# Optimization experiments

Hardware: AMD Instinct MI355X
Metric: run time of the kernel (lower is better)

The kernel has to match this reference:

```python
import jax, jax.numpy as jnp
import numpy as np

B, N, D_IN, D, E, MAXD = 16, 512, 256, 64, 32, 50
LN_EPS = 1e-5

def setup_inputs() -> dict:
    key = jax.random.key(0)
    ks = jax.random.split(key, 24)
    s = lambda fan: 1.0 / np.sqrt(fan)
    inp = {
        'x': jax.random.normal(ks[0], (B, N, D_IN), jnp.float32),
        'price_rising_ranks': jax.random.randint(ks[1], (B, N), 0, N, jnp.int64),
        'Wp': jax.random.normal(ks[2], (D_IN, D), jnp.float32) * s(D_IN),
        'bp': jnp.zeros((D,), jnp.float32),
        'Wq': jax.random.normal(ks[3], (D, D), jnp.float32) * s(D),
        'bq': jnp.zeros((D,), jnp.float32),
        'Wk': jax.random.normal(ks[4], (D, D), jnp.float32) * s(D),
        'bk': jnp.zeros((D,), jnp.float32),
        'Wv': jax.random.normal(ks[5], (D, D), jnp.float32) * s(D),
        'bv': jnp.zeros((D,), jnp.float32),
        'Eemb': jax.random.normal(ks[6], (MAXD + 1, E), jnp.float32),
        'Wr1': jax.random.normal(ks[7], (E, 16), jnp.float32) * s(E),
        'br1': jnp.zeros((16,), jnp.float32),
        'Wr2': jax.random.normal(ks[8], (16, 1), jnp.float32) * s(16),
        'Wf1': jax.random.normal(ks[9], (D, 2 * D), jnp.float32) * s(D),
        'bf1': jnp.zeros((2 * D,), jnp.float32),
        'Wf2': jax.random.normal(ks[10], (2 * D, D), jnp.float32) * s(2 * D),
        'bf2': jnp.zeros((D,), jnp.float32),
        'ln_g': jnp.ones((D,), jnp.float32),
        'ln_b': jnp.zeros((D,), jnp.float32),
        'Ws1': jax.random.normal(ks[11], (D, 32), jnp.float32) * s(D),
        'bs1': jnp.zeros((32,), jnp.float32),
        'Ws2': jax.random.normal(ks[12], (32, 1), jnp.float32) * s(32),
        'bs2': jnp.zeros((1,), jnp.float32),
    }
    return inp

def reference(x, price_rising_ranks, Wp, bp, Wq, bq, Wk, bk, Wv, bv,
              Eemb, Wr1, br1, Wr2, Wf1, bf1, Wf2, bf2, ln_g, ln_b,
              Ws1, bs1, Ws2, bs2):
    xp = x @ Wp + bp                                  # (B,N,D)
    q = xp @ Wq + bq
    k = xp @ Wk + bk
    v = xp @ Wv + bv
    scores = jnp.einsum('bnd,bmd->bnm', q, k) / jnp.sqrt(jnp.float32(D))
    # rank-distance pairwise bias
    r = price_rising_ranks
    dists = jnp.clip(jnp.abs(r[:, :, None] - r[:, None, :]), 0, MAXD)  # (B,N,N) int
    emb = Eemb[dists]                                 # (B,N,N,E)
    w = jax.nn.relu(emb @ Wr1 + br1) @ Wr2            # (B,N,N,1)
    rel = jax.nn.sigmoid(w[..., 0])                   # (B,N,N)
    scores = scores * rel
    attn = jax.nn.softmax(scores, axis=-1)
    ao = jnp.einsum('bnm,bmd->bnd', attn, v)
    # feed forward + layernorm
    h = jax.nn.relu(ao @ Wf1 + bf1) @ Wf2 + bf2
    mu = jnp.mean(h, axis=-1, keepdims=True)
    var = jnp.mean((h - mu) ** 2, axis=-1, keepdims=True)
    hn = (h - mu) / jnp.sqrt(var + LN_EPS) * ln_g + ln_b
    # score projection
    out = jax.nn.relu(hn @ Ws1 + bs1) @ Ws2 + bs2     # (B,N,1)
    return jax.nn.sigmoid(out[..., 0])                # (B,N)
```

## Files before the change

### kernel.cpp

```cpp
#include <hip/hip_runtime.h>

using f32x4 = __attribute__((ext_vector_type(4))) float;
using s16x8 = __attribute__((ext_vector_type(8))) short;

static __device__ __forceinline__ unsigned short f2bf(float f){
  union { float f; unsigned int i; } c; c.f = f;
  return (unsigned short)((c.i + 0x7FFFu + ((c.i >> 16) & 1u)) >> 16);
}
static __device__ __forceinline__ s16x8 ld8(const unsigned short* p){
  return *(const s16x8*)p;
}
static __device__ __forceinline__ s16x8 cvt8(const float* p){
  const float4* q = (const float4*)p;
  float4 a = q[0], b = q[1];
  s16x8 r;
  r[0]=(short)f2bf(a.x); r[1]=(short)f2bf(a.y); r[2]=(short)f2bf(a.z); r[3]=(short)f2bf(a.w);
  r[4]=(short)f2bf(b.x); r[5]=(short)f2bf(b.y); r[6]=(short)f2bf(b.z); r[7]=(short)f2bf(b.w);
  return r;
}
static __device__ __forceinline__ f32x4 mfma16(s16x8 a, s16x8 b, f32x4 c){
  return __builtin_amdgcn_mfma_f32_16x16x32_bf16(a, b, c, 0, 0, 0);
}

__global__ __launch_bounds__(128) void k_proj(const float* __restrict__ x,
    const float* __restrict__ Wp, const float* __restrict__ bp,
    const float* __restrict__ Wq, const float* __restrict__ bq,
    const float* __restrict__ Wk, const float* __restrict__ bk,
    const float* __restrict__ Wv, const float* __restrict__ bv,
    const float* __restrict__ Ee, const float* __restrict__ Wr1,
    const float* __restrict__ br1, const float* __restrict__ Wr2,
    unsigned short* __restrict__ q, unsigned short* __restrict__ kk,
    unsigned short* __restrict__ vt, float* __restrict__ rel_t)
{
  __shared__ __align__(16) unsigned short WpT[64*264];
  __shared__ __align__(16) unsigned short Wt3[3][64*72];
  __shared__ __align__(16) unsigned short xs[2][16*72];

  int t = threadIdx.x;
  for (int i = t; i < 256*64; i += 128){
    int k = i >> 6, n = i & 63;
    WpT[n*264 + k] = f2bf(Wp[i]);
  }
  for (int i = t; i < 64*64; i += 128){
    int k2 = i >> 6, n = i & 63;
    Wt3[0][n*72 + k2] = f2bf(Wq[i]);
    Wt3[1][n*72 + k2] = f2bf(Wk[i]);
    Wt3[2][n*72 + k2] = f2bf(Wv[i]);
  }
  if (blockIdx.x == 0 && t < 51){
    float e[32];
    for (int j = 0; j < 32; ++j) e[j] = Ee[t*32 + j];
    float w = 0.f;
    for (int h = 0; h < 16; ++h){
      float s = br1[h];
      for (int j = 0; j < 32; ++j) s += e[j] * Wr1[j*16 + h];
      w += fmaxf(s, 0.f) * Wr2[h];
    }
    rel_t[t] = 1.f / (1.f + __expf(-w));
  }
  __syncthreads();

  int lane = t & 63, wave = t >> 6, colL = lane & 15, quad = lane >> 4;
  int row0 = blockIdx.x*32 + wave*16;

  const float* xr = x + (row0 + colL)*256;
  f32x4 acc[4] = {};
  for (int kc = 0; kc < 256; kc += 32){
    s16x8 a = cvt8(xr + kc + quad*8);
#pragma unroll
    for (int nt = 0; nt < 4; ++nt)
      acc[nt] = mfma16(a, ld8(&WpT[(nt*16+colL)*264 + kc + quad*8]), acc[nt]);
  }
  unsigned short* xw = xs[wave];
#pragma unroll
  for (int nt = 0; nt < 4; ++nt){
    int col = nt*16 + colL;
    float bb = bp[col];
#pragma unroll
    for (int i = 0; i < 4; ++i)
      xw[(quad*4+i)*72 + col] = f2bf(acc[nt][i] + bb);
  }
  s16x8 a0 = ld8(&xw[colL*72 +  0 + quad*8]);
  s16x8 a1 = ld8(&xw[colL*72 + 32 + quad*8]);

#pragma unroll
  for (int w = 0; w < 3; ++w){
    const float* bias = w==0 ? bq : (w==1 ? bk : bv);
    f32x4 c[4] = {};
#pragma unroll
    for (int nt = 0; nt < 4; ++nt){
      c[nt] = mfma16(a0, ld8(&Wt3[w][(nt*16+colL)*72 +  0 + quad*8]), c[nt]);
      c[nt] = mfma16(a1, ld8(&Wt3[w][(nt*16+colL)*72 + 32 + quad*8]), c[nt]);
    }
#pragma unroll
    for (int nt = 0; nt < 4; ++nt){
      int col = nt*16 + colL;
      float bb = bias[col];
#pragma unroll
      for (int i = 0; i < 4; ++i){
        int row = row0 + quad*4 + i;
        float v = c[nt][i] + bb;
        if (w == 0)      q [row*64 + col] = f2bf(v);
        else if (w == 1) kk[row*64 + col] = f2bf(v);
        else             vt[(row>>9)*32768 + col*512 + (row & 511)] = f2bf(v);
      }
    }
  }
}

__global__ __launch_bounds__(256) void k_attn(const unsigned short* __restrict__ q,
    const unsigned short* __restrict__ kmat, const unsigned short* __restrict__ vt,
    const int* __restrict__ ranks, const float* __restrict__ rel_t,
    unsigned short* __restrict__ ao)
{
  int b = blockIdx.y, qt = blockIdx.x;
  int t = threadIdx.x, lane = t & 63, wave = t >> 6;
  int colL = lane & 15, quad = lane >> 4;

  __shared__ int r_s[512];
  __shared__ float rt_s[64];
  __shared__ __align__(16) unsigned short P[4][16*136];
  __shared__ float Opart[4][16*66];
  __shared__ float pmax_s[4][16], psum_s[4][16];

  for (int i = t; i < 512; i += 256) r_s[i] = ranks[b*512 + i];
  if (t < 64) rt_s[t] = (t < 51) ? rel_t[t] : 0.f;
  __syncthreads();

  int qrow0 = qt*16;
  const unsigned short* qp = q    + b*32768;
  const unsigned short* kp = kmat + b*32768;
  const unsigned short* vp = vt   + b*32768;

  s16x8 aq0 = ld8(qp + (qrow0+colL)*64 +  0 + quad*8);
  s16x8 aq1 = ld8(qp + (qrow0+colL)*64 + 32 + quad*8);

  int key0 = wave*128;
  f32x4 S[8];
#pragma unroll
  for (int mt = 0; mt < 8; ++mt){
    int key = key0 + mt*16 + colL;
    f32x4 c = {};
    c = mfma16(aq0, ld8(kp + key*64 +  0 + quad*8), c);
    c = mfma16(aq1, ld8(kp + key*64 + 32 + quad*8), c);
    S[mt] = c;
  }

  int rq[4];
#pragma unroll
  for (int i = 0; i < 4; ++i) rq[i] = r_s[qrow0 + quad*4 + i];

  float rmax[4] = {-1e30f,-1e30f,-1e30f,-1e30f};
#pragma unroll
  for (int mt = 0; mt < 8; ++mt){
    int rm = r_s[key0 + mt*16 + colL];
#pragma unroll
    for (int i = 0; i < 4; ++i){
      int dd = rq[i] - rm; dd = dd < 0 ? -dd : dd; dd = dd > 50 ? 50 : dd;
      float s = S[mt][i] * 0.125f * rt_s[dd];
      S[mt][i] = s;
      rmax[i] = fmaxf(rmax[i], s);
    }
  }
#pragma unroll
  for (int i = 0; i < 4; ++i){
    rmax[i] = fmaxf(rmax[i], __shfl_xor(rmax[i], 1));
    rmax[i] = fmaxf(rmax[i], __shfl_xor(rmax[i], 2));
    rmax[i] = fmaxf(rmax[i], __shfl_xor(rmax[i], 4));
    rmax[i] = fmaxf(rmax[i], __shfl_xor(rmax[i], 8));
  }
  if (colL == 0){
#pragma unroll
    for (int i = 0; i < 4; ++i) pmax_s[wave][quad*4 + i] = rmax[i];
  }
  __syncthreads();
  float gmax[4];
#pragma unroll
  for (int i = 0; i < 4; ++i){
    int r = quad*4 + i;
    gmax[i] = fmaxf(fmaxf(pmax_s[0][r], pmax_s[1][r]), fmaxf(pmax_s[2][r], pmax_s[3][r]));
  }
  float rsum[4] = {0.f,0.f,0.f,0.f};
#pragma unroll
  for (int mt = 0; mt < 8; ++mt){
#pragma unroll
    for (int i = 0; i < 4; ++i){
      float p = __expf(S[mt][i] - gmax[i]);
      S[mt][i] = p;
      rsum[i] += p;
    }
  }
#pragma unroll
  for (int i = 0; i < 4; ++i){
    rsum[i] += __shfl_xor(rsum[i], 1);
    rsum[i] += __shfl_xor(rsum[i], 2);
    rsum[i] += __shfl_xor(rsum[i], 4);
    rsum[i] += __shfl_xor(rsum[i], 8);
  }
  if (colL == 0){
#pragma unroll
    for (int i = 0; i < 4; ++i) psum_s[wave][quad*4 + i] = rsum[i];
  }
  __syncthreads();
  float inv[4];
#pragma unroll
  for (int i = 0; i < 4; ++i){
    int r = quad*4 + i;
    inv[i] = 1.f / (psum_s[0][r] + psum_s[1][r] + psum_s[2][r] + psum_s[3][r]);
  }
  unsigned short* Pw = P[wave];
#pragma unroll
  for (int mt = 0; mt < 8; ++mt){
#pragma unroll
    for (int i = 0; i < 4; ++i)
      Pw[(quad*4+i)*136 + mt*16 + colL] = f2bf(S[mt][i] * inv[i]);
  }
  f32x4 O[4] = {};
#pragma unroll
  for (int mc = 0; mc < 128; mc += 32){
    s16x8 ap = ld8(&Pw[colL*136 + mc + quad*8]);
#pragma unroll
    for (int dt = 0; dt < 4; ++dt)
      O[dt] = mfma16(ap, ld8(vp + (dt*16+colL)*512 + key0 + mc + quad*8), O[dt]);
  }
  float* Ow = Opart[wave];
#pragma unroll
  for (int dt = 0; dt < 4; ++dt)
#pragma unroll
    for (int i = 0; i < 4; ++i)
      Ow[(quad*4+i)*66 + dt*16 + colL] = O[dt][i];
  __syncthreads();
  for (int e = t; e < 1024; e += 256){
    int row = e >> 6, col = e & 63;
    float s = Opart[0][row*66+col] + Opart[1][row*66+col]
            + Opart[2][row*66+col] + Opart[3][row*66+col];
    ao[(b*512 + qrow0 + row)*64 + col] = f2bf(s);
  }
}

__global__ __launch_bounds__(128) void k_ffn(const unsigned short* __restrict__ ao,
    const float* __restrict__ Wf1, const float* __restrict__ bf1,
    const float* __restrict__ Wf2, const float* __restrict__ bf2,
    const float* __restrict__ lng, const float* __restrict__ lnb,
    const float* __restrict__ Ws1, const float* __restrict__ bs1,
    const float* __restrict__ Ws2, const float* __restrict__ bs2,
    float* __restrict__ out)
{
  __shared__ __align__(16) unsigned short Wf1t[128*72];
  __shared__ __align__(16) unsigned short Wf2t[64*136];
  __shared__ __align__(16) unsigned short Ws1t[32*72];
  __shared__ __align__(16) unsigned short hbuf[2][16*136];
  __shared__ float cb[384];

  int t = threadIdx.x;
  for (int i = t; i < 64*128; i += 128){ int d = i>>7, j = i&127; Wf1t[j*72 + d] = f2bf(Wf1[i]); }
  for (int i = t; i < 128*64; i += 128){ int kx = i>>6, n = i&63; Wf2t[n*136 + kx] = f2bf(Wf2[i]); }
  for (int i = t; i < 64*32;  i += 128){ int d = i>>5, c = i&31; Ws1t[c*72 + d] = f2bf(Ws1[i]); }
  if (t < 128) cb[t] = bf1[t];
  if (t < 64){ cb[128+t] = bf2[t]; cb[192+t] = lng[t]; cb[256+t] = lnb[t]; }
  if (t < 32){ cb[320+t] = bs1[t]; cb[352+t] = Ws2[t]; }
  __syncthreads();

  int lane = t & 63, wave = t >> 6, colL = lane & 15, quad = lane >> 4;
  int row0 = blockIdx.x*32 + wave*16;
  unsigned short* hw = hbuf[wave];

  f32x4 a1[8] = {};
#pragma unroll
  for (int kc = 0; kc < 64; kc += 32){
    s16x8 a = ld8(ao + (row0+colL)*64 + kc + quad*8);
#pragma unroll
    for (int nt = 0; nt < 8; ++nt)
      a1[nt] = mfma16(a, ld8(&Wf1t[(nt*16+colL)*72 + kc + quad*8]), a1[nt]);
  }
#pragma unroll
  for (int nt = 0; nt < 8; ++nt){
    int col = nt*16 + colL;
    float bb = cb[col];
#pragma unroll
    for (int i = 0; i < 4; ++i)
      hw[(quad*4+i)*136 + col] = f2bf(fmaxf(a1[nt][i] + bb, 0.f));
  }
  f32x4 a2[4] = {};
#pragma unroll
  for (int kc = 0; kc < 128; kc += 32){
    s16x8 a = ld8(&hw[colL*136 + kc + quad*8]);
#pragma unroll
    for (int nt = 0; nt < 4; ++nt)
      a2[nt] = mfma16(a, ld8(&Wf2t[(nt*16+colL)*136 + kc + quad*8]), a2[nt]);
  }
  float vals[4][4];
#pragma unroll
  for (int nt = 0; nt < 4; ++nt){
    float bb = cb[128 + nt*16 + colL];
#pragma unroll
    for (int i = 0; i < 4; ++i) vals[i][nt] = a2[nt][i] + bb;
  }
  float hnv[4][4];
#pragma unroll
  for (int i = 0; i < 4; ++i){
    float s = vals[i][0]+vals[i][1]+vals[i][2]+vals[i][3];
    s += __shfl_xor(s,1); s += __shfl_xor(s,2); s += __shfl_xor(s,4); s += __shfl_xor(s,8);
    float mu = s * (1.f/64.f);
    float d0=vals[i][0]-mu, d1=vals[i][1]-mu, d2=vals[i][2]-mu, d3=vals[i][3]-mu;
    float s2 = d0*d0 + d1*d1 + d2*d2 + d3*d3;
    s2 += __shfl_xor(s2,1); s2 += __shfl_xor(s2,2); s2 += __shfl_xor(s2,4); s2 += __shfl_xor(s2,8);
    float invs = rsqrtf(s2*(1.f/64.f) + 1e-5f);
#pragma unroll
    for (int nt = 0; nt < 4; ++nt){
      int col = nt*16 + colL;
      hnv[i][nt] = (vals[i][nt]-mu)*invs*cb[192+col] + cb[256+col];
    }
  }
#pragma unroll
  for (int i = 0; i < 4; ++i)
#pragma unroll
    for (int nt = 0; nt < 4; ++nt)
      hw[(quad*4+i)*72 + nt*16 + colL] = f2bf(hnv[i][nt]);

  f32x4 a3[2] = {};
#pragma unroll
  for (int kc = 0; kc < 64; kc += 32){
    s16x8 a = ld8(&hw[colL*72 + kc + quad*8]);
#pragma unroll
    for (int nt = 0; nt < 2; ++nt)
      a3[nt] = mfma16(a, ld8(&Ws1t[(nt*16+colL)*72 + kc + quad*8]), a3[nt]);
  }
  float bs2f = bs2[0];
#pragma unroll
  for (int i = 0; i < 4; ++i){
    float p = 0.f;
#pragma unroll
    for (int nt = 0; nt < 2; ++nt){
      int col = nt*16 + colL;
      p += fmaxf(a3[nt][i] + cb[320+col], 0.f) * cb[352+col];
    }
    p += __shfl_xor(p,1); p += __shfl_xor(p,2); p += __shfl_xor(p,4); p += __shfl_xor(p,8);
    if (colL == 0){
      float z = p + bs2f;
      out[row0 + quad*4 + i] = 1.f / (1.f + __expf(-z));
    }
  }
}

extern "C" void kernel_launch(void* const* d_in, const int* in_sizes, int n_in,
                              void* d_out, int out_size, void* d_ws, size_t ws_size,
                              hipStream_t stream)
{
  const float* x    = (const float*)d_in[0];
  const int*   rank = (const int*)d_in[1];
  const float* Wp   = (const float*)d_in[2];
  const float* bp   = (const float*)d_in[3];
  const float* Wq   = (const float*)d_in[4];
  const float* bq   = (const float*)d_in[5];
  const float* Wk   = (const float*)d_in[6];
  const float* bk   = (const float*)d_in[7];
  const float* Wv   = (const float*)d_in[8];
  const float* bv   = (const float*)d_in[9];
  const float* Ee   = (const float*)d_in[10];
  const float* Wr1  = (const float*)d_in[11];
  const float* br1  = (const float*)d_in[12];
  const float* Wr2  = (const float*)d_in[13];
  const float* Wf1  = (const float*)d_in[14];
  const float* bf1  = (const float*)d_in[15];
  const float* Wf2  = (const float*)d_in[16];
  const float* bf2  = (const float*)d_in[17];
  const float* lng  = (const float*)d_in[18];
  const float* lnb  = (const float*)d_in[19];
  const float* Ws1  = (const float*)d_in[20];
  const float* bs1  = (const float*)d_in[21];
  const float* Ws2  = (const float*)d_in[22];
  const float* bs2  = (const float*)d_in[23];
  float* out = (float*)d_out;

  char* ws = (char*)d_ws;
  float*          rel_t = (float*)(ws + 0);
  unsigned short* q     = (unsigned short*)(ws + 256);
  unsigned short* kk    = (unsigned short*)(ws + 256 + 1*1048576);
  unsigned short* vt    = (unsigned short*)(ws + 256 + 2*1048576);
  unsigned short* ao    = (unsigned short*)(ws + 256 + 3*1048576);

  k_proj<<<dim3(256), dim3(128), 0, stream>>>(x, Wp, bp, Wq, bq, Wk, bk, Wv, bv,
                                              Ee, Wr1, br1, Wr2, q, kk, vt, rel_t);
  k_attn<<<dim3(32, 16), dim3(256), 0, stream>>>(q, kk, vt, rank, rel_t, ao);
  k_ffn<<<dim3(256), dim3(128), 0, stream>>>(ao, Wf1, bf1, Wf2, bf2, lng, lnb,
                                             Ws1, bs1, Ws2, bs2, out);
}
```

Before: 147.3 us.

## Fuse FFN, layernorm and score head into the attention kernel

Removes the separate FFN kernel launch. Each attention block now keeps its 16-row output tile in LDS and runs the FFN, layernorm and score projection on it directly, so the bf16 attention output no longer goes through global memory. The FFN weights are converted to bf16 once in k_proj, in a pre-transposed layout, so every fused block can copy them into LDS with vector loads. In exchange, LDS use per block grows a lot, which may lower occupancy, and all 4 waves repeat the same FFN math on the same tile.

```diff
diff --git a/kernel.cpp b/kernel.cpp
--- a/kernel.cpp
+++ b/kernel.cpp
@@ -29,8 +29,12 @@
     const float* __restrict__ Wv, const float* __restrict__ bv,
     const float* __restrict__ Ee, const float* __restrict__ Wr1,
     const float* __restrict__ br1, const float* __restrict__ Wr2,
+    const float* __restrict__ Wf1, const float* __restrict__ Wf2,
+    const float* __restrict__ Ws1,
     unsigned short* __restrict__ q, unsigned short* __restrict__ kk,
-    unsigned short* __restrict__ vt, float* __restrict__ rel_t)
+    unsigned short* __restrict__ vt, float* __restrict__ rel_t,
+    unsigned short* __restrict__ Wf1p, unsigned short* __restrict__ Wf2p,
+    unsigned short* __restrict__ Ws1p)
 {
   __shared__ __align__(16) unsigned short WpT[64*264];
   __shared__ __align__(16) unsigned short Wt3[3][64*72];
@@ -58,6 +62,12 @@
     }
     rel_t[t] = 1.f / (1.f + __expf(-w));
   }
+  if (blockIdx.x == 1)
+    for (int i = t; i < 64*128; i += 128){ int d = i>>7, n = i&127; Wf1p[n*64 + d] = f2bf(Wf1[i]); }
+  if (blockIdx.x == 2)
+    for (int i = t; i < 128*64; i += 128){ int k2 = i>>6, n = i&63; Wf2p[n*128 + k2] = f2bf(Wf2[i]); }
+  if (blockIdx.x == 3)
+    for (int i = t; i < 64*32;  i += 128){ int d = i>>5, c = i&31; Ws1p[c*64 + d] = f2bf(Ws1[i]); }
   __syncthreads();
 
   int lane = t & 63, wave = t >> 6, colL = lane & 15, quad = lane >> 4;
@@ -108,10 +118,15 @@
   }
 }
 
-__global__ __launch_bounds__(256) void k_attn(const unsigned short* __restrict__ q,
+__global__ __launch_bounds__(256) void k_attn_ffn(const unsigned short* __restrict__ q,
     const unsigned short* __restrict__ kmat, const unsigned short* __restrict__ vt,
     const int* __restrict__ ranks, const float* __restrict__ rel_t,
-    unsigned short* __restrict__ ao)
+    const unsigned short* __restrict__ Wf1p, const unsigned short* __restrict__ Wf2p,
+    const unsigned short* __restrict__ Ws1p,
+    const float* __restrict__ bf1, const float* __restrict__ bf2,
+    const float* __restrict__ lng, const float* __restrict__ lnb,
+    const float* __restrict__ bs1, const float* __restrict__ Ws2,
+    const float* __restrict__ bs2, float* __restrict__ out)
 {
   int b = blockIdx.y, qt = blockIdx.x;
   int t = threadIdx.x, lane = t & 63, wave = t >> 6;
@@ -119,12 +134,30 @@
 
   __shared__ int r_s[512];
   __shared__ float rt_s[64];
+  __shared__ float pmax_s[4][16], psum_s[4][16];
+  __shared__ __align__(16) unsigned short Wf1t[128*72];
+  __shared__ __align__(16) unsigned short Wf2t[64*136];
+  __shared__ __align__(16) unsigned short Ws1t[32*72];
   __shared__ __align__(16) unsigned short P[4][16*136];
-  __shared__ float Opart[4][16*66];
-  __shared__ float pmax_s[4][16], psum_s[4][16];
+  __shared__ __align__(16) unsigned short aot[16*72];
+  __shared__ float Opart[4][16*65];
+  __shared__ float cb[384];
 
   for (int i = t; i < 512; i += 256) r_s[i] = ranks[b*512 + i];
   if (t < 64) rt_s[t] = (t < 51) ? rel_t[t] : 0.f;
+  for (int i = t; i < 1024; i += 256){ int r = i>>3, c = i&7;  *(s16x8*)&Wf1t[r*72  + c*8] = ld8(Wf1p + r*64  + c*8); }
+  for (int i = t; i < 1024; i += 256){ int r = i>>4, c = i&15; *(s16x8*)&Wf2t[r*136 + c*8] = ld8(Wf2p + r*128 + c*8); }
+  { int i = t; if (i < 256){ int r = i>>3, c = i&7; *(s16x8*)&Ws1t[r*72 + c*8] = ld8(Ws1p + r*64 + c*8); } }
+  for (int i = t; i < 384; i += 256){
+    float v;
+    if      (i < 128) v = bf1[i];
+    else if (i < 192) v = bf2[i-128];
+    else if (i < 256) v = lng[i-192];
+    else if (i < 320) v = lnb[i-256];
+    else if (i < 352) v = bs1[i-320];
+    else              v = Ws2[i-352];
+    cb[i] = v;
+  }
   __syncthreads();
 
   int qrow0 = qt*16;
@@ -228,51 +261,25 @@
   for (int dt = 0; dt < 4; ++dt)
 #pragma unroll
     for (int i = 0; i < 4; ++i)
-      Ow[(quad*4+i)*66 + dt*16 + colL] = O[dt][i];
+      Ow[(quad*4+i)*65 + dt*16 + colL] = O[dt][i];
   __syncthreads();
   for (int e = t; e < 1024; e += 256){
     int row = e >> 6, col = e & 63;
-    float s = Opart[0][row*66+col] + Opart[1][row*66+col]
-            + Opart[2][row*66+col] + Opart[3][row*66+col];
-    ao[(b*512 + qrow0 + row)*64 + col] = f2bf(s);
-  }
-}
-
-__global__ __launch_bounds__(128) void k_ffn(const unsigned short* __restrict__ ao,
-    const float* __restrict__ Wf1, const float* __restrict__ bf1,
-    const float* __restrict__ Wf2, const float* __restrict__ bf2,
-    const float* __restrict__ lng, const float* __restrict__ lnb,
-    const float* __restrict__ Ws1, const float* __restrict__ bs1,
-    const float* __restrict__ Ws2, const float* __restrict__ bs2,
-    float* __restrict__ out)
-{
-  __shared__ __align__(16) unsigned short Wf1t[128*72];
-  __shared__ __align__(16) unsigned short Wf2t[64*136];
-  __shared__ __align__(16) unsigned short Ws1t[32*72];
-  __shared__ __align__(16) unsigned short hbuf[2][16*136];
-  __shared__ float cb[384];
-
-  int t = threadIdx.x;
-  for (int i = t; i < 64*128; i += 128){ int d = i>>7, j = i&127; Wf1t[j*72 + d] = f2bf(Wf1[i]); }
-  for (int i = t; i < 128*64; i += 128){ int kx = i>>6, n = i&63; Wf2t[n*136 + kx] = f2bf(Wf2[i]); }
-  for (int i = t; i < 64*32;  i += 128){ int d = i>>5, c = i&31; Ws1t[c*72 + d] = f2bf(Ws1[i]); }
-  if (t < 128) cb[t] = bf1[t];
-  if (t < 64){ cb[128+t] = bf2[t]; cb[192+t] = lng[t]; cb[256+t] = lnb[t]; }
-  if (t < 32){ cb[320+t] = bs1[t]; cb[352+t] = Ws2[t]; }
-  __syncthreads();
-
-  int lane = t & 63, wave = t >> 6, colL = lane & 15, quad = lane >> 4;
-  int row0 = blockIdx.x*32 + wave*16;
-  unsigned short* hw = hbuf[wave];
+    float s = Opart[0][row*65+col] + Opart[1][row*65+col]
+            + Opart[2][row*65+col] + Opart[3][row*65+col];
+    aot[row*72 + col] = f2bf(s);
+  }
+  __syncthreads();
 
   f32x4 a1[8] = {};
 #pragma unroll
   for (int kc = 0; kc < 64; kc += 32){
-    s16x8 a = ld8(ao + (row0+colL)*64 + kc + quad*8);
+    s16x8 a = ld8(&aot[colL*72 + kc + quad*8]);
 #pragma unroll
     for (int nt = 0; nt < 8; ++nt)
       a1[nt] = mfma16(a, ld8(&Wf1t[(nt*16+colL)*72 + kc + quad*8]), a1[nt]);
   }
+  unsigned short* hw = Pw;
 #pragma unroll
   for (int nt = 0; nt < 8; ++nt){
     int col = nt*16 + colL;
@@ -318,27 +325,29 @@
     for (int nt = 0; nt < 4; ++nt)
       hw[(quad*4+i)*72 + nt*16 + colL] = f2bf(hnv[i][nt]);
 
-  f32x4 a3[2] = {};
-#pragma unroll
-  for (int kc = 0; kc < 64; kc += 32){
-    s16x8 a = ld8(&hw[colL*72 + kc + quad*8]);
-#pragma unroll
-    for (int nt = 0; nt < 2; ++nt)
-      a3[nt] = mfma16(a, ld8(&Ws1t[(nt*16+colL)*72 + kc + quad*8]), a3[nt]);
-  }
-  float bs2f = bs2[0];
-#pragma unroll
-  for (int i = 0; i < 4; ++i){
-    float p = 0.f;
-#pragma unroll
-    for (int nt = 0; nt < 2; ++nt){
-      int col = nt*16 + colL;
-      p += fmaxf(a3[nt][i] + cb[320+col], 0.f) * cb[352+col];
-    }
-    p += __shfl_xor(p,1); p += __shfl_xor(p,2); p += __shfl_xor(p,4); p += __shfl_xor(p,8);
-    if (colL == 0){
-      float z = p + bs2f;
-      out[row0 + quad*4 + i] = 1.f / (1.f + __expf(-z));
+  if (wave == 0){
+    f32x4 a3[2] = {};
+#pragma unroll
+    for (int kc = 0; kc < 64; kc += 32){
+      s16x8 a = ld8(&hw[colL*72 + kc + quad*8]);
+#pragma unroll
+      for (int nt = 0; nt < 2; ++nt)
+        a3[nt] = mfma16(a, ld8(&Ws1t[(nt*16+colL)*72 + kc + quad*8]), a3[nt]);
+    }
+    float bs2f = bs2[0];
+#pragma unroll
+    for (int i = 0; i < 4; ++i){
+      float p = 0.f;
+#pragma unroll
+      for (int nt = 0; nt < 2; ++nt){
+        int col = nt*16 + colL;
+        p += fmaxf(a3[nt][i] + cb[320+col], 0.f) * cb[352+col];
+      }
+      p += __shfl_xor(p,1); p += __shfl_xor(p,2); p += __shfl_xor(p,4); p += __shfl_xor(p,8);
+      if (colL == 0){
+        float z = p + bs2f;
+        out[b*512 + qrow0 + quad*4 + i] = 1.f / (1.f + __expf(-z));
+      }
     }
   }
 }
@@ -375,14 +384,17 @@
 
   char* ws = (char*)d_ws;
   float*          rel_t = (float*)(ws + 0);
-  unsigned short* q     = (unsigned short*)(ws + 256);
-  unsigned short* kk    = (unsigned short*)(ws + 256 + 1*1048576);
-  unsigned short* vt    = (unsigned short*)(ws + 256 + 2*1048576);
-  unsigned short* ao    = (unsigned short*)(ws + 256 + 3*1048576);
+  unsigned short* Wf1p  = (unsigned short*)(ws + 4096);
+  unsigned short* Wf2p  = (unsigned short*)(ws + 4096 + 16384);
+  unsigned short* Ws1p  = (unsigned short*)(ws + 4096 + 32768);
+  unsigned short* q     = (unsigned short*)(ws + 65536);
+  unsigned short* kk    = (unsigned short*)(ws + 65536 + 1*1048576);
+  unsigned short* vt    = (unsigned short*)(ws + 65536 + 2*1048576);
 
   k_proj<<<dim3(256), dim3(128), 0, stream>>>(x, Wp, bp, Wq, bq, Wk, bk, Wv, bv,
-                                              Ee, Wr1, br1, Wr2, q, kk, vt, rel_t);
-  k_attn<<<dim3(32, 16), dim3(256), 0, stream>>>(q, kk, vt, rank, rel_t, ao);
-  k_ffn<<<dim3(256), dim3(128), 0, stream>>>(ao, Wf1, bf1, Wf2, bf2, lng, lnb,
-                                             Ws1, bs1, Ws2, bs2, out);
-}
+                                              Ee, Wr1, br1, Wr2, Wf1, Wf2, Ws1,
+                                              q, kk, vt, rel_t, Wf1p, Wf2p, Ws1p);
+  k_attn_ffn<<<dim3(32, 16), dim3(256), 0, stream>>>(q, kk, vt, rank, rel_t,
+                                                     Wf1p, Wf2p, Ws1p,
+                                                     bf1, bf2, lng, lnb, bs1, Ws2, bs2, out);
+}
```

Result: no change. 149.2 us (+1.3%).
